# Performance work log

Hardware: AMD Instinct MI355X
Metric: run time of the kernel (lower is better)

## Reference

```python
import jax, jax.numpy as jnp
import numpy as np

RADIUS = 2  # module init kwarg


def _lga(cost, weights, r):
    """One local-guided-aggregation pass.
    cost:    [B, D, H, W]
    weights: [B, 3*K*K, H, W], K = 2r+1; group 0/1/2 weight disparity d-1/d/d+1.
    """
    B, D, H, W = cost.shape
    K = 2 * r + 1
    # zero-pad: disparity by 1 (for d-1 / d+1), spatial by r (window)
    cp = jnp.pad(cost, ((0, 0), (1, 1), (r, r), (r, r)))
    w = weights.reshape(B, 3, K * K, H, W)
    out = jnp.zeros_like(cost)
    for idx in range(K * K):
        i, j = idx // K, idx % K
        # window view: cp[:, :, y+i, x+j] == cost[:, :, y+i-r, x+j-r]
        win = cp[:, :, i:i + H, j:j + W]          # [B, D+2, H, W]
        out = out + (w[:, 0, idx][:, None] * win[:, 0:D]        # cost[d-1]
                     + w[:, 1, idx][:, None] * win[:, 1:D + 1]  # cost[d]
                     + w[:, 2, idx][:, None] * win[:, 2:D + 2]) # cost[d+1]
    return out


def setup_inputs() -> dict:
    key = jax.random.key(0)
    k1, k2 = jax.random.split(key)
    B, D, H, W = 2, 64, 384, 768
    K = 2 * RADIUS + 1
    input1 = jax.random.normal(k1, (B, D, H, W), dtype=jnp.float32)
    # aggregation stays numerically tame (mimics normalized guidance)
    input2 = jax.random.uniform(k2, (B, 3 * K * K, H, W), dtype=jnp.float32) * (1.0 / (3 * K * K))
    return {"input1": input1, "input2": input2}


def reference(input1, input2):
    out = input1
    for _ in range(3):  # LGA3 = three sequential LGA passes, same weights
        out = _lga(out, input2, RADIUS)
    return out
```

## Files before the change

kernel.cpp:

```cpp
#include <hip/hip_runtime.h>


#define B_ 2
#define D_ 64
#define H_ 384
#define W_ 768
static constexpr int HW    = H_ * W_;
static constexpr int DPT   = 8;
static constexpr int NTY   = 4;
static constexpr int WT    = 64;
static constexpr int HSEG  = 8;
static constexpr int RITER = HSEG + 4;
static constexpr int LROW  = 72;
static constexpr int LRWS  = 34;
static constexpr int NGRAN = LRWS * 18;
static constexpr int NCH_C = 10;
static constexpr int NCH_W = 19;
static constexpr int WCH   = 76;

__device__ __forceinline__ void gld_lds16(const float* g, float* l) {
  __builtin_amdgcn_global_load_lds((const __attribute__((address_space(1))) unsigned int*)g,
                                   (__attribute__((address_space(3))) unsigned int*)l,
                                   16, 0, 0);
}

__global__ __launch_bounds__(256, 1) void lga_pass(const float* __restrict__ src,
                                                   const float* __restrict__ wts,
                                                   float* __restrict__ dst) {
  __shared__ float cl[NCH_C * 256];
  __shared__ float wl[WCH * 64];

  const int tx    = threadIdx.x;
  const int ty    = threadIdx.y;
  const int bx    = blockIdx.x;
  const int w0    = bx * WT, w = w0 + tx;
  const int hs    = blockIdx.y * HSEG;
  const int b     = blockIdx.z >> 1;
  const int dhalf = blockIdx.z & 1;
  const int dbase = dhalf * 32 - 1;
  const int d0    = dhalf * 32 + ty * DPT;

  const float* sb  = src + (size_t)b * D_ * HW;
  const float* wtb = wts + (size_t)b * 75 * HW;

  const bool has_lo = (d0 > 0);
  const bool has_hi = (d0 + DPT < D_);
  const bool edge   = (bx == 0) || (bx == W_ / WT - 1);

  float acc[5][DPT];
#pragma unroll
  for (int s = 0; s < 5; ++s)
#pragma unroll
    for (int k = 0; k < DPT; ++k) acc[s][k] = 0.f;

#pragma unroll 1
  for (int r = 0; r < RITER; ++r) {
    {
      int h_in = hs - 2 + r;
      h_in = h_in < 0 ? 0 : (h_in >= H_ ? H_ - 1 : h_in);
#pragma unroll
      for (int q = 0; q < 3; ++q) {
        const int c = ty + q * 4;
        if (c < NCH_C) {
          int G = c * 64 + tx;
          G = G > NGRAN - 1 ? NGRAN - 1 : G;
          const int p = G / 18;
          const int k = G - p * 18;
          int pd = dbase + p;
          pd = pd < 0 ? 0 : (pd > D_ - 1 ? D_ - 1 : pd);
          long idx = (long)pd * HW + (long)h_in * W_ + (w0 - 4) + (k << 2);
          idx = idx < 0 ? 0 : idx;
          const long mx = (long)D_ * HW - 4;
          idx = idx > mx ? mx : idx;
          gld_lds16(sb + idx, &cl[c * 256]);
        }
      }
    }
    {
#pragma unroll
      for (int q = 0; q < 5; ++q) {
        const int ci = ty + q * 4;
        if (ci < NCH_W) {
          int ch = ci * 4 + (tx >> 4);
          ch = ch > 74 ? 74 : ch;
          const int s  = ch / 15;
          const int t  = ch - s * 15;
          const int g  = t / 5;
          const int j  = t - g * 5;
          const int cw = (4 - s) * 5 + j + g * 25;
          int o = hs + r - 4 + s;
          o = o < 0 ? 0 : (o >= H_ ? H_ - 1 : o);
          const float* p = wtb + (size_t)cw * HW + (size_t)o * W_ + w0 + ((tx & 15) << 2);
          gld_lds16(p, &wl[ci * 256]);
        }
      }
    }

    __syncthreads();

    const int  h_in = hs - 2 + r;
    const bool hv   = (unsigned)h_in < (unsigned)H_;
    float vv[5][DPT + 2];
    if (hv) {
      const float* vbase = cl + ty * DPT * LROW + tx + 2;
      if (!edge) {
#pragma unroll
        for (int j = 0; j < 5; ++j)
#pragma unroll
          for (int m = 0; m < DPT + 2; ++m)
            vv[j][m] = vbase[m * LROW + j];
        if (!has_lo) {
#pragma unroll
          for (int j = 0; j < 5; ++j) vv[j][0] = 0.f;
        }
        if (!has_hi) {
#pragma unroll
          for (int j = 0; j < 5; ++j) vv[j][DPT + 1] = 0.f;
        }
      } else {
#pragma unroll
        for (int j = 0; j < 5; ++j) {
          const bool wokj = (unsigned)(w + j - 2) < (unsigned)W_;
#pragma unroll
          for (int m = 0; m < DPT + 2; ++m) {
            const float v = vbase[m * LROW + j];
            bool ok = wokj;
            if (m == 0)       ok = ok && has_lo;
            if (m == DPT + 1) ok = ok && has_hi;
            vv[j][m] = ok ? v : 0.f;
          }
        }
      }
    }

#pragma unroll
    for (int s = 0; s < 5; ++s) {
      if (hv && (unsigned)(r - 4 + s) < (unsigned)HSEG) {
        const float* wsl = wl + s * 15 * 64 + tx;
#pragma unroll
        for (int j = 0; j < 5; ++j) {
          const float w0v = wsl[(j)      * 64];
          const float w1v = wsl[(5 + j)  * 64];
          const float w2v = wsl[(10 + j) * 64];
#pragma unroll
          for (int k = 0; k < DPT; ++k)
            acc[s][k] = fmaf(w0v, vv[j][k],
                        fmaf(w1v, vv[j][k + 1],
                        fmaf(w2v, vv[j][k + 2], acc[s][k])));
        }
      }
    }

    if (r >= 4) {
      const int o = hs + r - 4;
#pragma unroll
      for (int k = 0; k < DPT; ++k) {
        float* dp = dst + (((size_t)b * D_ + d0 + k) * H_ + o) * W_;
        dp[w] = acc[0][k];
      }
    }

#pragma unroll
    for (int s = 0; s < 4; ++s)
#pragma unroll
      for (int k = 0; k < DPT; ++k) acc[s][k] = acc[s + 1][k];
#pragma unroll
    for (int k = 0; k < DPT; ++k) acc[4][k] = 0.f;

    __syncthreads();
  }
}

extern "C" void kernel_launch(void* const* d_in, const int* in_sizes, int n_in,
                              void* d_out, int out_size, void* d_ws, size_t ws_size,
                              hipStream_t stream) {
  const float* cost = (const float*)d_in[0];
  const float* wts  = (const float*)d_in[1];
  float* out = (float*)d_out;
  float* ws  = (float*)d_ws;

  dim3 grid(W_ / WT, H_ / HSEG, B_ * 2);
  dim3 block(WT, NTY);

  lga_pass<<<grid, block, 0, stream>>>(cost, wts, out);
  lga_pass<<<grid, block, 0, stream>>>(out, wts, ws);
  lga_pass<<<grid, block, 0, stream>>>(ws, wts, out);
}
```

Measured before the change: 552.4 us.

## Double-buffer weight tiles and prefetch next cost row to overlap loads with compute

Weights now go into two LDS buffers, and the next row's weight tile is issued right after the barrier. The next cost row is prefetched into the single cost buffer as soon as the current row has been read into registers. The two full __syncthreads per iteration are replaced by manual s_waitcnt vmcnt and s_barrier plus sched_barrier, so global-to-LDS transfers can overlap the FMA work. The hand-tuned vmcnt counts and the removed channel guards (the buffers are enlarged to fit) make the code fragile if the load counts change.

```diff
diff --git a/kernel.cpp b/kernel.cpp
--- a/kernel.cpp
+++ b/kernel.cpp
@@ -11,12 +11,13 @@
 static constexpr int WT    = 64;
 static constexpr int HSEG  = 8;
 static constexpr int RITER = HSEG + 4;
-static constexpr int LROW  = 72;
+static constexpr int PLW   = 72;
 static constexpr int LRWS  = 34;
 static constexpr int NGRAN = LRWS * 18;
-static constexpr int NCH_C = 10;
-static constexpr int NCH_W = 19;
-static constexpr int WCH   = 76;
+static constexpr int NCH_C = 12;
+static constexpr int NCH_W = 20;
+static constexpr int CLF   = NCH_C * 256;
+static constexpr int WLF   = NCH_W * 256;
 
 __device__ __forceinline__ void gld_lds16(const float* g, float* l) {
   __builtin_amdgcn_global_load_lds((const __attribute__((address_space(1))) unsigned int*)g,
@@ -27,8 +28,8 @@
 __global__ __launch_bounds__(256, 1) void lga_pass(const float* __restrict__ src,
                                                    const float* __restrict__ wts,
                                                    float* __restrict__ dst) {
-  __shared__ float cl[NCH_C * 256];
-  __shared__ float wl[WCH * 64];
+  __shared__ float cl[CLF];
+  __shared__ float wl[2][WLF];
 
   const int tx    = threadIdx.x;
   const int ty    = threadIdx.y;
@@ -47,6 +48,47 @@
   const bool has_hi = (d0 + DPT < D_);
   const bool edge   = (bx == 0) || (bx == W_ / WT - 1);
 
+  auto stage_c = [&](int h_in) {
+#pragma unroll
+    for (int q = 0; q < 3; ++q) {
+      const int c = ty + q * 4;
+      int G = c * 64 + tx;
+      G = G > NGRAN - 1 ? NGRAN - 1 : G;
+      const int p = G / 18;
+      const int k = G - p * 18;
+      int pd = dbase + p;
+      pd = pd < 0 ? 0 : (pd > D_ - 1 ? D_ - 1 : pd);
+      long idx = (long)pd * HW + (long)h_in * W_ + (w0 - 4) + (k << 2);
+      idx = idx < 0 ? 0 : idx;
+      const long mx = (long)D_ * HW - 4;
+      idx = idx > mx ? mx : idx;
+      gld_lds16(sb + idx, &cl[c * 256]);
+    }
+  };
+
+  auto stage_w = [&](int rr) {
+#pragma unroll
+    for (int q = 0; q < 5; ++q) {
+      const int ci = ty + q * 4;
+      int ch = ci * 4 + (tx >> 4);
+      ch = ch > 74 ? 74 : ch;
+      const int s  = ch / 15;
+      const int t  = ch - s * 15;
+      const int g  = t / 5;
+      const int j  = t - g * 5;
+      const int cw = (4 - s) * 5 + j + g * 25;
+      int o = hs + rr - 4 + s;
+      o = o < 0 ? 0 : (o >= H_ ? H_ - 1 : o);
+      const float* p = wtb + (size_t)cw * HW + (size_t)o * W_ + w0 + ((tx & 15) << 2);
+      gld_lds16(p, &wl[rr & 1][ci * 256]);
+    }
+  };
+
+  auto clampH = [](int h) { return h < 0 ? 0 : (h >= H_ ? H_ - 1 : h); };
+
+  stage_w(0);
+  stage_c(clampH(hs - 2));
+
   float acc[5][DPT];
 #pragma unroll
   for (int s = 0; s < 5; ++s)
@@ -55,60 +97,24 @@
 
 #pragma unroll 1
   for (int r = 0; r < RITER; ++r) {
-    {
-      int h_in = hs - 2 + r;
-      h_in = h_in < 0 ? 0 : (h_in >= H_ ? H_ - 1 : h_in);
-#pragma unroll
-      for (int q = 0; q < 3; ++q) {
-        const int c = ty + q * 4;
-        if (c < NCH_C) {
-          int G = c * 64 + tx;
-          G = G > NGRAN - 1 ? NGRAN - 1 : G;
-          const int p = G / 18;
-          const int k = G - p * 18;
-          int pd = dbase + p;
-          pd = pd < 0 ? 0 : (pd > D_ - 1 ? D_ - 1 : pd);
-          long idx = (long)pd * HW + (long)h_in * W_ + (w0 - 4) + (k << 2);
-          idx = idx < 0 ? 0 : idx;
-          const long mx = (long)D_ * HW - 4;
-          idx = idx > mx ? mx : idx;
-          gld_lds16(sb + idx, &cl[c * 256]);
-        }
-      }
-    }
-    {
-#pragma unroll
-      for (int q = 0; q < 5; ++q) {
-        const int ci = ty + q * 4;
-        if (ci < NCH_W) {
-          int ch = ci * 4 + (tx >> 4);
-          ch = ch > 74 ? 74 : ch;
-          const int s  = ch / 15;
-          const int t  = ch - s * 15;
-          const int g  = t / 5;
-          const int j  = t - g * 5;
-          const int cw = (4 - s) * 5 + j + g * 25;
-          int o = hs + r - 4 + s;
-          o = o < 0 ? 0 : (o >= H_ ? H_ - 1 : o);
-          const float* p = wtb + (size_t)cw * HW + (size_t)o * W_ + w0 + ((tx & 15) << 2);
-          gld_lds16(p, &wl[ci * 256]);
-        }
-      }
-    }
+    if (r <= 4) { asm volatile("s_waitcnt vmcnt(0)" ::: "memory"); }
+    else        { asm volatile("s_waitcnt vmcnt(8)" ::: "memory"); }
+    __builtin_amdgcn_s_barrier();
+    __builtin_amdgcn_sched_barrier(0);
 
-    __syncthreads();
+    if (r + 1 < RITER) stage_w(r + 1);
 
     const int  h_in = hs - 2 + r;
     const bool hv   = (unsigned)h_in < (unsigned)H_;
     float vv[5][DPT + 2];
     if (hv) {
-      const float* vbase = cl + ty * DPT * LROW + tx + 2;
+      const float* vb = cl + ty * DPT * PLW + tx + 2;
       if (!edge) {
 #pragma unroll
         for (int j = 0; j < 5; ++j)
 #pragma unroll
           for (int m = 0; m < DPT + 2; ++m)
-            vv[j][m] = vbase[m * LROW + j];
+            vv[j][m] = vb[m * PLW + j];
         if (!has_lo) {
 #pragma unroll
           for (int j = 0; j < 5; ++j) vv[j][0] = 0.f;
@@ -123,7 +129,7 @@
           const bool wokj = (unsigned)(w + j - 2) < (unsigned)W_;
 #pragma unroll
           for (int m = 0; m < DPT + 2; ++m) {
-            const float v = vbase[m * LROW + j];
+            const float v = vb[m * PLW + j];
             bool ok = wokj;
             if (m == 0)       ok = ok && has_lo;
             if (m == DPT + 1) ok = ok && has_hi;
@@ -133,10 +139,17 @@
       }
     }
 
+    asm volatile("s_waitcnt lgkmcnt(0)" ::: "memory");
+    __builtin_amdgcn_s_barrier();
+    __builtin_amdgcn_sched_barrier(0);
+
+    if (r + 1 < RITER) stage_c(clampH(hs - 2 + r + 1));
+
+    const float* wcur = wl[r & 1];
 #pragma unroll
     for (int s = 0; s < 5; ++s) {
       if (hv && (unsigned)(r - 4 + s) < (unsigned)HSEG) {
-        const float* wsl = wl + s * 15 * 64 + tx;
+        const float* wsl = wcur + s * 15 * 64 + tx;
 #pragma unroll
         for (int j = 0; j < 5; ++j) {
           const float w0v = wsl[(j)      * 64];
@@ -166,8 +179,6 @@
       for (int k = 0; k < DPT; ++k) acc[s][k] = acc[s + 1][k];
 #pragma unroll
     for (int k = 0; k < DPT; ++k) acc[4][k] = 0.f;
-
-    __syncthreads();
   }
 }
 
```

After: 594.5 us. 1.08x slower.
